# Performance work log

Hardware: AMD Instinct MI355X
Metric: run time of the kernel (lower is better)

The kernel has to match this reference:

```python
import jax, jax.numpy as jnp
import numpy as np

B, C_IN, H, W = 4, 256, 64, 64
LATENT = 256


def setup_inputs() -> dict:
    key = jax.random.key(0)
    ks = jax.random.split(key, 12)
    s_in = 1.0 / np.sqrt(C_IN)
    s_lat = 1.0 / np.sqrt(LATENT)
    return {
        "x": jax.random.normal(ks[0], (B, C_IN, H, W), dtype=jnp.float32),
        # 1x1 conv weights stored as [out, in]
        "wq": jax.random.normal(ks[1], (LATENT, C_IN), dtype=jnp.float32) * s_in,
        "bq": jnp.zeros((LATENT,), dtype=jnp.float32),
        "wk": jax.random.normal(ks[2], (LATENT, C_IN), dtype=jnp.float32) * s_in,
        "bk": jnp.zeros((LATENT,), dtype=jnp.float32),
        "wv": jax.random.normal(ks[3], (LATENT, C_IN), dtype=jnp.float32) * s_in,
        "bv": jnp.zeros((LATENT,), dtype=jnp.float32),
        "w_out": jax.random.normal(ks[4], (C_IN, LATENT), dtype=jnp.float32) * s_lat,
        "b_out": jnp.zeros((C_IN,), dtype=jnp.float32),
        # positional-embedding MLP (torch nn.Linear: y = x @ W.T + b)
        "mlp_w1": jax.random.normal(ks[5], (LATENT, LATENT), dtype=jnp.float32) * s_lat,
        "mlp_b1": jnp.zeros((LATENT,), dtype=jnp.float32),
        "mlp_w2": jax.random.normal(ks[6], (LATENT, LATENT), dtype=jnp.float32) * s_lat,
        "mlp_b2": jnp.zeros((LATENT,), dtype=jnp.float32),
    }


def _sinusoidal_table(timesteps, dim):
    # embed[t, d] = sin(arg) if d even else cos(arg), arg = t / 10000**(2d/dim)
    t = jnp.arange(timesteps, dtype=jnp.float32)[:, None]
    p = jnp.arange(dim, dtype=jnp.float32)[None, :]
    w = t / jnp.power(jnp.float32(10000.0), 2.0 * p / dim)
    even = (jnp.arange(dim) % 2 == 0)[None, :]
    return jnp.where(even, jnp.sin(w), jnp.cos(w))  # [T, dim]


def _conv1x1(x, w, b):
    # x: [B, Cin, H, W], w: [Cout, Cin]
    return jnp.einsum('bchw,oc->bohw', x, w) + b[None, :, None, None]


def reference(x, wq, bq, wk, bk, wv, bv, w_out, b_out, mlp_w1, mlp_b1, mlp_w2, mlp_b2):
    batch, _, h, w_ = x.shape
    L = wq.shape[0]
    hw = h * w_

    q = _conv1x1(x, wq, bq)
    k = _conv1x1(x, wk, bk)
    v = _conv1x1(x, wv, bv)

    pe = _sinusoidal_table(hw, L)                     # [HW, L]
    pe = jax.nn.silu(pe @ mlp_w1.T + mlp_b1) @ mlp_w2.T + mlp_b2
    pe = pe.reshape(1, L, h, w_)                      # faithful to torch reshape

    q = (q + pe).reshape(batch, L, hw)
    k = (k + pe).reshape(batch, L, hw)
    v = (v + pe).reshape(batch, L, hw)

    # attention[b, i, j] = sum_c q[b, c, i] * k[b, c, j] / sqrt(L)
    att = jnp.einsum('bci,bcj->bij', q, k) / jnp.sqrt(jnp.float32(L))
    att = jax.nn.softmax(att, axis=1)                 # SAGAN-style: softmax over queries
    res = jnp.einsum('bci,bij->bcj', v, att)          # bmm(v, attention)
    res = res.reshape(batch, L, h, w_)
    return _conv1x1(res, w_out, b_out)
```

## Files before the change

kernel.cpp:

```cpp
#include <hip/hip_runtime.h>
#include <cstdint>


typedef short s8v __attribute__((ext_vector_type(8)));
typedef float f32x4 __attribute__((ext_vector_type(4)));
typedef unsigned int u32x2 __attribute__((ext_vector_type(2)));
typedef unsigned int u32x4 __attribute__((ext_vector_type(4)));

#define DEVI static __device__ __forceinline__

DEVI unsigned short f2bf(float f) {
  union { float f; uint32_t u; } x; x.f = f;
  uint32_t u = x.u;
  return (unsigned short)((u + 0x7fffu + ((u >> 16) & 1u)) >> 16);
}

DEVI void pl32swap(uint32_t& a, uint32_t& b) {
#if __has_builtin(__builtin_amdgcn_permlane32_swap)
  u32x2 r = __builtin_amdgcn_permlane32_swap(a, b, false, false);
  a = r[0]; b = r[1];
#else
  asm("v_permlane32_swap_b32 %0, %1" : "+v"(a), "+v"(b));
#endif
}

DEVI void gl_lds16(const void* g, void* l) {
  __builtin_amdgcn_global_load_lds(
      (const __attribute__((address_space(1))) void*)g,
      (__attribute__((address_space(3))) void*)l,
      16, 0, 0);
}

DEVI void stage(const unsigned short* src, int ld, unsigned short* lds, int t) {
  gl_lds16(src + (long)(t >> 2) * ld + (t & 3) * 8, lds + (t >> 6) * 512);
}

template <int OBF, int BIAS, int PEM, int SILU>
__global__ __launch_bounds__(256) void gemm_nt(
    const unsigned short* __restrict__ A, const unsigned short* __restrict__ B,
    void* __restrict__ Cp, int K, int N, int ld, long sA, long sB, long sC,
    const float* __restrict__ bias, const float* __restrict__ pe, float scale) {
  const int bz = blockIdx.z;
  const unsigned short* Ab = A + (long)bz * sA;
  const unsigned short* Bb = B + (long)bz * sB;
  const int m0 = blockIdx.x * 128, n0 = blockIdx.y * 128;
  __shared__ __align__(16) unsigned short As[4096], Bs[4096];
  const int t = threadIdx.x;
  const int wave = t >> 6, lane = t & 63;
  const int wr = wave >> 1, wc = wave & 1;

  f32x4 acc[4][4];
#pragma unroll
  for (int i = 0; i < 4; i++)
#pragma unroll
    for (int j = 0; j < 4; j++) acc[i][j] = f32x4{0.f, 0.f, 0.f, 0.f};

  const int rl = lane & 15, kp = (lane >> 4) * 8;

  for (int k0 = 0; k0 < K; k0 += 32) {
    stage(Ab + (long)m0 * ld + k0, ld, As, t);
    stage(Ab + (long)(m0 + 64) * ld + k0, ld, As + 2048, t);
    stage(Bb + (long)n0 * ld + k0, ld, Bs, t);
    stage(Bb + (long)(n0 + 64) * ld + k0, ld, Bs + 2048, t);
    __syncthreads();

    s8v af[4], bfr[4];
#pragma unroll
    for (int i = 0; i < 4; i++)
      af[i] = *(const s8v*)(As + (wr * 64 + i * 16 + rl) * 32 + kp);
#pragma unroll
    for (int j = 0; j < 4; j++)
      bfr[j] = *(const s8v*)(Bs + (wc * 64 + j * 16 + rl) * 32 + kp);
#pragma unroll
    for (int i = 0; i < 4; i++)
#pragma unroll
      for (int j = 0; j < 4; j++)
        acc[i][j] = __builtin_amdgcn_mfma_f32_16x16x32_bf16(af[i], bfr[j],
                                                            acc[i][j], 0, 0, 0);
    __syncthreads();
  }

  const long cb = (long)bz * sC;
#pragma unroll
  for (int i = 0; i < 4; i++) {
    const int r0 = m0 + wr * 64 + i * 16 + (lane >> 4) * 4;
#pragma unroll
    for (int j = 0; j < 4; j++) {
      const int col = n0 + wc * 64 + j * 16 + (lane & 15);
#pragma unroll
      for (int r = 0; r < 4; r++) {
        const int row = r0 + r;
        float val = acc[i][j][r] * scale;
        if (BIAS == 1) val += bias[row];
        if (BIAS == 2) val += bias[col];
        if (PEM == 1) val += pe[(long)row * 4096 + col];
        if (PEM == 2) val += pe[(long)col * 4096 + row];
        if (SILU) val = val / (1.0f + __expf(-val));
        const long ci = cb + (long)row * N + col;
        if (OBF)
          ((unsigned short*)Cp)[ci] = f2bf(val);
        else
          ((float*)Cp)[ci] = val;
      }
    }
  }
}

__global__ __launch_bounds__(512) void gemm_qkv(
    const unsigned short* __restrict__ XT, const unsigned short* __restrict__ wqb,
    const unsigned short* __restrict__ wkb, const unsigned short* __restrict__ wvb,
    unsigned short* __restrict__ qT, unsigned short* __restrict__ kT,
    unsigned short* __restrict__ vB, const float* __restrict__ bq,
    const float* __restrict__ bk, const float* __restrict__ bv,
    const float* __restrict__ pe) {
  const int bz = blockIdx.z;
  const unsigned short* Ab = XT + (long)bz * 1048576;
  const int m0 = blockIdx.x * 128, n0 = blockIdx.y * 128;
  __shared__ __align__(16) unsigned short As[4096], Bq[4096], Bk[4096],
      Bv[4096];
  const int t = threadIdx.x;
  const int wave = t >> 6, lane = t & 63;
  const int wm = wave >> 2, wn = wave & 3;
  const int rl = lane & 15, kp = (lane >> 4) * 8;
  const int th = t >> 8, tt = t & 255;

  f32x4 aq[4][2], ak[4][2], av[4][2];
#pragma unroll
  for (int i = 0; i < 4; i++)
#pragma unroll
    for (int j = 0; j < 2; j++) {
      aq[i][j] = f32x4{0.f, 0.f, 0.f, 0.f};
      ak[i][j] = f32x4{0.f, 0.f, 0.f, 0.f};
      av[i][j] = f32x4{0.f, 0.f, 0.f, 0.f};
    }

  for (int k0 = 0; k0 < 256; k0 += 32) {
    const long ro = (long)(th * 64) * 256 + k0;
    stage(Ab + (long)m0 * 256 + ro, 256, As + th * 2048, tt);
    stage(wqb + (long)n0 * 256 + ro, 256, Bq + th * 2048, tt);
    stage(wkb + (long)n0 * 256 + ro, 256, Bk + th * 2048, tt);
    stage(wvb + (long)n0 * 256 + ro, 256, Bv + th * 2048, tt);
    __syncthreads();

    s8v af[4], b0[2], b1[2], b2[2];
#pragma unroll
    for (int i = 0; i < 4; i++)
      af[i] = *(const s8v*)(As + (wm * 64 + i * 16 + rl) * 32 + kp);
#pragma unroll
    for (int j = 0; j < 2; j++) {
      b0[j] = *(const s8v*)(Bq + (wn * 32 + j * 16 + rl) * 32 + kp);
      b1[j] = *(const s8v*)(Bk + (wn * 32 + j * 16 + rl) * 32 + kp);
      b2[j] = *(const s8v*)(Bv + (wn * 32 + j * 16 + rl) * 32 + kp);
    }
#pragma unroll
    for (int i = 0; i < 4; i++)
#pragma unroll
      for (int j = 0; j < 2; j++) {
        aq[i][j] = __builtin_amdgcn_mfma_f32_16x16x32_bf16(af[i], b0[j],
                                                           aq[i][j], 0, 0, 0);
        ak[i][j] = __builtin_amdgcn_mfma_f32_16x16x32_bf16(af[i], b1[j],
                                                           ak[i][j], 0, 0, 0);
        av[i][j] = __builtin_amdgcn_mfma_f32_16x16x32_bf16(af[i], b2[j],
                                                           av[i][j], 0, 0, 0);
      }
    __syncthreads();
  }

  const long cb = (long)bz * 1048576;
#pragma unroll
  for (int i = 0; i < 4; i++) {
    const int row0 = m0 + wm * 64 + i * 16 + (lane >> 4) * 4;
#pragma unroll
    for (int j = 0; j < 2; j++) {
      const int col = n0 + wn * 32 + j * 16 + rl;
      const float4 p4 = *(const float4*)(pe + (long)col * 4096 + row0);
      const float bqc = bq[col], bkc = bk[col], bvc = bv[col];
      ushort4 vpk;
      const float pv[4] = {p4.x, p4.y, p4.z, p4.w};
#pragma unroll
      for (int r = 0; r < 4; r++) {
        const int row = row0 + r;
        qT[cb + (long)row * 256 + col] = f2bf(aq[i][j][r] + bqc + pv[r]);
        kT[cb + (long)row * 256 + col] = f2bf(ak[i][j][r] + bkc + pv[r]);
      }
      vpk.x = f2bf(av[i][j][0] + bvc + pv[0]);
      vpk.y = f2bf(av[i][j][1] + bvc + pv[1]);
      vpk.z = f2bf(av[i][j][2] + bvc + pv[2]);
      vpk.w = f2bf(av[i][j][3] + bvc + pv[3]);
      *(ushort4*)(vB + cb + (long)col * 4096 + row0) = vpk;
    }
  }
}

__global__ __launch_bounds__(256) void gemm_out_f(
    const unsigned short* __restrict__ wob, const float* __restrict__ oPart,
    const float* __restrict__ lPart, const float* __restrict__ bo,
    float* __restrict__ out) {
  const int bz = blockIdx.z;
  const int m0 = blockIdx.x * 128, n0 = blockIdx.y * 128;
  __shared__ __align__(16) unsigned short As[4096], Bs[4096];
  const int t = threadIdx.x;
  const int wave = t >> 6, lane = t & 63;
  const int wr = wave >> 1, wc = wave & 1;

  f32x4 acc[4][4];
#pragma unroll
  for (int i = 0; i < 4; i++)
#pragma unroll
    for (int j = 0; j < 4; j++) acc[i][j] = f32x4{0.f, 0.f, 0.f, 0.f};

  const int rl = lane & 15, kp = (lane >> 4) * 8;
  const int tr = t >> 2, tc8 = (t & 3) * 8;

  const int j0_ = n0 + tr, j1_ = n0 + 64 + tr;
  const float* l0p = lPart + (long)(bz * 2) * 4096;
  const float* l1p = lPart + (long)(bz * 2 + 1) * 4096;
  const float inv0 = 1.0f / (l0p[j0_] + l1p[j0_]);
  const float inv1 = 1.0f / (l0p[j1_] + l1p[j1_]);
  const float* oP0 = oPart + (long)(bz * 2) * 1048576;
  const float* oP1 = oPart + (long)(bz * 2 + 1) * 1048576;

  for (int k0 = 0; k0 < 256; k0 += 32) {
    stage(wob + (long)m0 * 256 + k0, 256, As, t);
    stage(wob + (long)(m0 + 64) * 256 + k0, 256, As + 2048, t);
#pragma unroll
    for (int h = 0; h < 2; h++) {
      const int j = h ? j1_ : j0_;
      const float inv = h ? inv1 : inv0;
      const float4* a4 = (const float4*)(oP0 + (long)j * 256 + k0 + tc8);
      const float4* d4 = (const float4*)(oP1 + (long)j * 256 + k0 + tc8);
      const float4 a0 = a4[0], a1 = a4[1], d0 = d4[0], d1 = d4[1];
      s8v pk;
      pk[0] = (short)f2bf((a0.x + d0.x) * inv);
      pk[1] = (short)f2bf((a0.y + d0.y) * inv);
      pk[2] = (short)f2bf((a0.z + d0.z) * inv);
      pk[3] = (short)f2bf((a0.w + d0.w) * inv);
      pk[4] = (short)f2bf((a1.x + d1.x) * inv);
      pk[5] = (short)f2bf((a1.y + d1.y) * inv);
      pk[6] = (short)f2bf((a1.z + d1.z) * inv);
      pk[7] = (short)f2bf((a1.w + d1.w) * inv);
      *(s8v*)(Bs + h * 2048 + tr * 32 + tc8) = pk;
    }
    __syncthreads();

    s8v af[4], bfr[4];
#pragma unroll
    for (int i = 0; i < 4; i++)
      af[i] = *(const s8v*)(As + (wr * 64 + i * 16 + rl) * 32 + kp);
#pragma unroll
    for (int j = 0; j < 4; j++)
      bfr[j] = *(const s8v*)(Bs + (wc * 64 + j * 16 + rl) * 32 + kp);
#pragma unroll
    for (int i = 0; i < 4; i++)
#pragma unroll
      for (int j = 0; j < 4; j++)
        acc[i][j] = __builtin_amdgcn_mfma_f32_16x16x32_bf16(af[i], bfr[j],
                                                            acc[i][j], 0, 0, 0);
    __syncthreads();
  }

  const long cb = (long)bz * 1048576;
#pragma unroll
  for (int i = 0; i < 4; i++) {
    const int r0 = m0 + wr * 64 + i * 16 + (lane >> 4) * 4;
#pragma unroll
    for (int j = 0; j < 4; j++) {
      const int col = n0 + wc * 64 + j * 16 + (lane & 15);
#pragma unroll
      for (int r = 0; r < 4; r++) {
        const int row = r0 + r;
        out[cb + (long)row * 4096 + col] = acc[i][j][r] + bo[row];
      }
    }
  }
}

__global__ __launch_bounds__(512, 2) void flash_attn(
    const unsigned short* __restrict__ qTp, const unsigned short* __restrict__ kTp,
    const unsigned short* __restrict__ vBp, float* __restrict__ oPart,
    float* __restrict__ lPart) {
  const int bid = blockIdx.x;
  const int xcd = bid & 7;
  const int b = xcd >> 1, ihalf = xcd & 1;
  const int j0 = (bid >> 3) * 128;
  const long S = 1048576;
  const long ibase = (long)ihalf * 2048;
  const unsigned short* q = qTp + (long)b * S;
  const unsigned short* k = kTp + (long)b * S;
  const unsigned short* v = vBp + (long)b * S;
  const int ob = b * 2 + ihalf;

  __shared__ __align__(16) unsigned char ldsb[131584];

  const int t = threadIdx.x;
  const int wave = t >> 6, lane = t & 63;
  const int jq = wave & 3, ch = wave >> 2;
  const int rl = lane & 15, g = lane >> 4;
  const int kp = g * 8;
  const int ksw = ((g ^ ((rl >> 1) & 3)) << 3);
  const int qrow = (rl & 3) | ((rl & 4) << 1) | ((rl & 8) >> 1);
  const int kswq = ((g ^ ((qrow >> 1) & 3)) << 3);
  const int th = t >> 8, tt = t & 255;

  const unsigned short* krow = k + (long)(j0 + jq * 32 + rl) * 256 + kp;
  s8v kreg[2][8];
#pragma unroll
  for (int jf = 0; jf < 2; jf++)
#pragma unroll
    for (int s = 0; s < 8; s++)
      kreg[jf][s] = *(const s8v*)(krow + jf * 16 * 256 + s * 32);

  f32x4 oacc[16][2];
#pragma unroll
  for (int cf = 0; cf < 16; cf++)
#pragma unroll
    for (int jf = 0; jf < 2; jf++) oacc[cf][jf] = f32x4{0.f, 0.f, 0.f, 0.f};
  float plsum[2] = {0.f, 0.f};

  const int tr = tt >> 2, tc = tt & 3;
  const int sc = (tc ^ ((tr >> 1) & 3)) * 8;
  const unsigned short* qsrc[4];
  const unsigned short* vsrc[4];
  const int dsto = (tt >> 6) * 512;
#pragma unroll
  for (int ss = 0; ss < 4; ss++) {
    const int s_ = ss * 2 + th;
    qsrc[ss] = q + ibase * 256 + s_ * 32 + (long)tr * 256 + sc;
    vsrc[ss] = v + (long)((s_ >> 1) * 64) * 4096 + ibase + (s_ & 1) * 32 +
               (long)tr * 4096 + sc;
  }

#define STAGE_QV(bufsel)                                                     \
  {                                                                          \
    unsigned short* qD = (unsigned short*)(ldsb + ((bufsel) << 15));         \
    unsigned short* vD = (unsigned short*)(ldsb + 65536 + ((bufsel) << 15)); \
    _Pragma("unroll") for (int ss = 0; ss < 4; ss++) {                       \
      const int s_ = ss * 2 + th;                                            \
      gl_lds16(qsrc[ss], qD + s_ * 2048 + dsto);                             \
      gl_lds16(vsrc[ss], vD + s_ * 2048 + dsto);                             \
      qsrc[ss] += 16384;                                                     \
      vsrc[ss] += 64;                                                        \
    }                                                                        \
  }

  STAGE_QV(0)

  for (int n = 0; n < 32; ++n) {
    const int cur = n & 1;
    __syncthreads();
    STAGE_QV(cur ^ 1)

    f32x4 sa[2][2];
#pragma unroll
    for (int kk = 0; kk < 2; kk++)
#pragma unroll
      for (int jf = 0; jf < 2; jf++) sa[kk][jf] = f32x4{0.f, 0.f, 0.f, 0.f};
    const unsigned short* qbase =
        (const unsigned short*)(ldsb + (cur << 15)) +
        (ch * 32 + qrow) * 32 + kswq;
#pragma unroll
    for (int s = 0; s < 8; s++) {
      s8v qf0 = *(const s8v*)(qbase + s * 2048);
      s8v qf1 = *(const s8v*)(qbase + s * 2048 + 512);
      sa[0][0] = __builtin_amdgcn_mfma_f32_16x16x32_bf16(qf0, kreg[0][s],
                                                         sa[0][0], 0, 0, 0);
      sa[0][1] = __builtin_amdgcn_mfma_f32_16x16x32_bf16(qf0, kreg[1][s],
                                                         sa[0][1], 0, 0, 0);
      sa[1][0] = __builtin_amdgcn_mfma_f32_16x16x32_bf16(qf1, kreg[0][s],
                                                         sa[1][0], 0, 0, 0);
      sa[1][1] = __builtin_amdgcn_mfma_f32_16x16x32_bf16(qf1, kreg[1][s],
                                                         sa[1][1], 0, 0, 0);
    }

    uint32_t pd[2][2][2];
#pragma unroll
    for (int kk = 0; kk < 2; kk++)
#pragma unroll
      for (int jf = 0; jf < 2; jf++) {
        const float p0 = exp2f(sa[kk][jf][0] * 0.09016844005556021f);
        const float p1 = exp2f(sa[kk][jf][1] * 0.09016844005556021f);
        const float p2 = exp2f(sa[kk][jf][2] * 0.09016844005556021f);
        const float p3 = exp2f(sa[kk][jf][3] * 0.09016844005556021f);
        plsum[jf] += (p0 + p1) + (p2 + p3);
        pd[kk][jf][0] = (uint32_t)f2bf(p0) | ((uint32_t)f2bf(p1) << 16);
        pd[kk][jf][1] = (uint32_t)f2bf(p2) | ((uint32_t)f2bf(p3) << 16);
      }

    s8v pB[2];
#pragma unroll
    for (int jf = 0; jf < 2; jf++) {
      uint32_t a0 = pd[0][jf][0], b0 = pd[1][jf][0];
      uint32_t a1 = pd[0][jf][1], b1 = pd[1][jf][1];
      pl32swap(a0, b0);
      pl32swap(a1, b1);
      u32x4 w4 = {a0, a1, b0, b1};
      pB[jf] = __builtin_bit_cast(s8v, w4);
    }

    const unsigned short* vbase =
        (const unsigned short*)(ldsb + 65536 + (cur << 15)) + ch * 2048 +
        rl * 32 + ksw;
#pragma unroll
    for (int cf = 0; cf < 16; cf++) {
      s8v vb = *(const s8v*)(vbase + (cf >> 2) * 4096 + (cf & 3) * 512);
      oacc[cf][0] = __builtin_amdgcn_mfma_f32_16x16x32_bf16(vb, pB[0],
                                                            oacc[cf][0], 0, 0, 0);
      oacc[cf][1] = __builtin_amdgcn_mfma_f32_16x16x32_bf16(vb, pB[1],
                                                            oacc[cf][1], 0, 0, 0);
    }
  }

#pragma unroll
  for (int jf = 0; jf < 2; jf++) {
    plsum[jf] += __shfl_xor(plsum[jf], 16);
    plsum[jf] += __shfl_xor(plsum[jf], 32);
  }

  __syncthreads();
  float4* ex = (float4*)ldsb;
  float* exl = (float*)(ldsb + 131072);
  if (ch == 1) {
#pragma unroll
    for (int jf = 0; jf < 2; jf++) {
#pragma unroll
      for (int cf = 0; cf < 16; cf++)
        ex[jq * 2048 + (jf * 16 + rl) * 64 + cf * 4 + g] =
            float4{oacc[cf][jf][0], oacc[cf][jf][1], oacc[cf][jf][2],
                   oacc[cf][jf][3]};
      if (g == 0) exl[jq * 32 + jf * 16 + rl] = plsum[jf];
    }
  }
  __syncthreads();
  if (ch == 0) {
    float4* op4 = (float4*)(oPart + (long)ob * 1048576);
#pragma unroll
    for (int jf = 0; jf < 2; jf++) {
      const int jl = jq * 32 + jf * 16 + rl;
      if (g == 0)
        lPart[(long)ob * 4096 + j0 + jl] = plsum[jf] + exl[jl];
#pragma unroll
      for (int cf = 0; cf < 16; cf++) {
        const float4 o = ex[jq * 2048 + (jf * 16 + rl) * 64 + cf * 4 + g];
        op4[(long)(j0 + jl) * 64 + cf * 4 + g] =
            float4{oacc[cf][jf][0] + o.x, oacc[cf][jf][1] + o.y,
                   oacc[cf][jf][2] + o.z, oacc[cf][jf][3] + o.w};
      }
    }
  }
#undef STAGE_QV
}

__global__ __launch_bounds__(256) void prep_all(
    const float* __restrict__ a0, const float* __restrict__ a1,
    const float* __restrict__ a2, const float* __restrict__ a3,
    const float* __restrict__ a4, const float* __restrict__ a5,
    unsigned short* __restrict__ wdst, unsigned short* __restrict__ emb,
    const float* __restrict__ x, unsigned short* __restrict__ xt) {
  __shared__ float tile[32][33];
  const int bid = blockIdx.x;
  const int t = threadIdx.x;
  if (bid < 1536) {
    int idx = bid * 256 + t;
    int m = idx >> 16, r = idx & 65535;
    const float* s;
    switch (m) {
      case 0: s = a0; break;
      case 1: s = a1; break;
      case 2: s = a2; break;
      case 3: s = a3; break;
      case 4: s = a4; break;
      default: s = a5; break;
    }
    wdst[idx] = f2bf(s[r]);
  } else if (bid < 5632) {
    int idx = (bid - 1536) * 256 + t;
    int tt_ = idx >> 8, d = idx & 255;
    float freq = exp2f((float)d * -0.10381025296573598f);
    float w = (float)tt_ * freq;
    float sn, cs;
    __sincosf(w, &sn, &cs);
    emb[idx] = f2bf((d & 1) ? cs : sn);
  } else {
    const int bid2 = bid - 5632;
    const int s0 = (bid2 & 127) * 32, c0 = ((bid2 >> 7) & 7) * 32;
    const int b = bid2 >> 10;
    const int tx = t & 31, ty = t >> 5;
    const float* xb = x + (long)b * 256 * 4096;
#pragma unroll
    for (int r = 0; r < 32; r += 8)
      tile[ty + r][tx] = xb[(long)(c0 + ty + r) * 4096 + s0 + tx];
    __syncthreads();
    unsigned short* xtb = xt + (long)b * 4096 * 256;
#pragma unroll
    for (int r = 0; r < 32; r += 8)
      xtb[(long)(s0 + ty + r) * 256 + c0 + tx] = f2bf(tile[tx][ty + r]);
  }
}

extern "C" void kernel_launch(void* const* d_in, const int* in_sizes, int n_in,
                              void* d_out, int out_size, void* d_ws,
                              size_t ws_size, hipStream_t stream) {
  const float* x  = (const float*)d_in[0];
  const float* wq = (const float*)d_in[1];
  const float* bq = (const float*)d_in[2];
  const float* wk = (const float*)d_in[3];
  const float* bk = (const float*)d_in[4];
  const float* wv = (const float*)d_in[5];
  const float* bv = (const float*)d_in[6];
  const float* wo = (const float*)d_in[7];
  const float* bo = (const float*)d_in[8];
  const float* w1 = (const float*)d_in[9];
  const float* b1 = (const float*)d_in[10];
  const float* w2 = (const float*)d_in[11];
  const float* b2 = (const float*)d_in[12];
  float* out = (float*)d_out;

  char* ws = (char*)d_ws;
  unsigned short* wqb = (unsigned short*)(ws + 0);
  unsigned short* wkb = (unsigned short*)(ws + 131072);
  unsigned short* wvb = (unsigned short*)(ws + 262144);
  unsigned short* wob = (unsigned short*)(ws + 393216);
  unsigned short* w1b = (unsigned short*)(ws + 524288);
  unsigned short* w2b = (unsigned short*)(ws + 655360);
  unsigned short* emb = (unsigned short*)(ws + 786432);
  unsigned short* h1b = (unsigned short*)(ws + 2883584);
  float*          peF = (float*)(ws + 4980736);
  unsigned short* XT  = (unsigned short*)(ws + 9175040);
  unsigned short* qT  = (unsigned short*)(ws + 17563648);
  unsigned short* kT  = (unsigned short*)(ws + 25952256);
  unsigned short* vB  = (unsigned short*)(ws + 34340864);
  float*          oP  = (float*)(ws + 51118080);
  float*          lP  = (float*)(ws + 84672512);
  (void)ws_size; (void)in_sizes; (void)n_in; (void)out_size;

  const dim3 B256(256);

  prep_all<<<9728, B256, 0, stream>>>(wq, wk, wv, wo, w1, w2, wqb, emb, x, XT);
  gemm_nt<1, 2, 0, 1><<<dim3(32, 2, 1), B256, 0, stream>>>(
      emb, w1b, h1b, 256, 256, 256, 0, 0, 0, b1, nullptr, 1.0f);
  gemm_nt<0, 2, 0, 0><<<dim3(32, 2, 1), B256, 0, stream>>>(
      h1b, w2b, peF, 256, 256, 256, 0, 0, 0, b2, nullptr, 1.0f);
  gemm_qkv<<<dim3(32, 2, 4), dim3(512), 0, stream>>>(
      XT, wqb, wkb, wvb, qT, kT, vB, bq, bk, bv, peF);
  flash_attn<<<256, dim3(512), 0, stream>>>(qT, kT, vB, oP, lP);
  gemm_out_f<<<dim3(2, 32, 4), B256, 0, stream>>>(wob, oP, lP, bo, out);
}
```

Baseline: 148.6 us.

## Route attention probabilities through LDS instead of permlane swaps; retile output GEMM

```diff
diff --git a/kernel.cpp b/kernel.cpp
--- a/kernel.cpp
+++ b/kernel.cpp
@@ -4,8 +4,6 @@
 
 typedef short s8v __attribute__((ext_vector_type(8)));
 typedef float f32x4 __attribute__((ext_vector_type(4)));
-typedef unsigned int u32x2 __attribute__((ext_vector_type(2)));
-typedef unsigned int u32x4 __attribute__((ext_vector_type(4)));
 
 #define DEVI static __device__ __forceinline__
 
@@ -13,15 +11,6 @@
   union { float f; uint32_t u; } x; x.f = f;
   uint32_t u = x.u;
   return (unsigned short)((u + 0x7fffu + ((u >> 16) & 1u)) >> 16);
-}
-
-DEVI void pl32swap(uint32_t& a, uint32_t& b) {
-#if __has_builtin(__builtin_amdgcn_permlane32_swap)
-  u32x2 r = __builtin_amdgcn_permlane32_swap(a, b, false, false);
-  a = r[0]; b = r[1];
-#else
-  asm("v_permlane32_swap_b32 %0, %1" : "+v"(a), "+v"(b));
-#endif
 }
 
 DEVI void gl_lds16(const void* g, void* l) {
@@ -197,38 +186,33 @@
     const float* __restrict__ lPart, const float* __restrict__ bo,
     float* __restrict__ out) {
   const int bz = blockIdx.z;
-  const int m0 = blockIdx.x * 128, n0 = blockIdx.y * 128;
-  __shared__ __align__(16) unsigned short As[4096], Bs[4096];
+  const int n0 = blockIdx.y * 64;
+  __shared__ __align__(16) unsigned short As[8192], Bs[2048];
   const int t = threadIdx.x;
   const int wave = t >> 6, lane = t & 63;
-  const int wr = wave >> 1, wc = wave & 1;
-
-  f32x4 acc[4][4];
-#pragma unroll
-  for (int i = 0; i < 4; i++)
-#pragma unroll
-    for (int j = 0; j < 4; j++) acc[i][j] = f32x4{0.f, 0.f, 0.f, 0.f};
-
   const int rl = lane & 15, kp = (lane >> 4) * 8;
   const int tr = t >> 2, tc8 = (t & 3) * 8;
 
-  const int j0_ = n0 + tr, j1_ = n0 + 64 + tr;
+  f32x4 acc[4][4];
+#pragma unroll
+  for (int i = 0; i < 4; i++)
+#pragma unroll
+    for (int j = 0; j < 4; j++) acc[i][j] = f32x4{0.f, 0.f, 0.f, 0.f};
+
+  const int j_ = n0 + tr;
   const float* l0p = lPart + (long)(bz * 2) * 4096;
   const float* l1p = lPart + (long)(bz * 2 + 1) * 4096;
-  const float inv0 = 1.0f / (l0p[j0_] + l1p[j0_]);
-  const float inv1 = 1.0f / (l0p[j1_] + l1p[j1_]);
+  const float inv = 1.0f / (l0p[j_] + l1p[j_]);
   const float* oP0 = oPart + (long)(bz * 2) * 1048576;
   const float* oP1 = oPart + (long)(bz * 2 + 1) * 1048576;
 
   for (int k0 = 0; k0 < 256; k0 += 32) {
-    stage(wob + (long)m0 * 256 + k0, 256, As, t);
-    stage(wob + (long)(m0 + 64) * 256 + k0, 256, As + 2048, t);
-#pragma unroll
-    for (int h = 0; h < 2; h++) {
-      const int j = h ? j1_ : j0_;
-      const float inv = h ? inv1 : inv0;
-      const float4* a4 = (const float4*)(oP0 + (long)j * 256 + k0 + tc8);
-      const float4* d4 = (const float4*)(oP1 + (long)j * 256 + k0 + tc8);
+#pragma unroll
+    for (int s_ = 0; s_ < 4; s_++)
+      stage(wob + (long)(s_ * 64) * 256 + k0, 256, As + s_ * 2048, t);
+    {
+      const float4* a4 = (const float4*)(oP0 + (long)j_ * 256 + k0 + tc8);
+      const float4* d4 = (const float4*)(oP1 + (long)j_ * 256 + k0 + tc8);
       const float4 a0 = a4[0], a1 = a4[1], d0 = d4[0], d1 = d4[1];
       s8v pk;
       pk[0] = (short)f2bf((a0.x + d0.x) * inv);
@@ -239,17 +223,17 @@
       pk[5] = (short)f2bf((a1.y + d1.y) * inv);
       pk[6] = (short)f2bf((a1.z + d1.z) * inv);
       pk[7] = (short)f2bf((a1.w + d1.w) * inv);
-      *(s8v*)(Bs + h * 2048 + tr * 32 + tc8) = pk;
+      *(s8v*)(Bs + tr * 32 + tc8) = pk;
     }
     __syncthreads();
 
     s8v af[4], bfr[4];
 #pragma unroll
     for (int i = 0; i < 4; i++)
-      af[i] = *(const s8v*)(As + (wr * 64 + i * 16 + rl) * 32 + kp);
+      af[i] = *(const s8v*)(As + (wave * 64 + i * 16 + rl) * 32 + kp);
 #pragma unroll
     for (int j = 0; j < 4; j++)
-      bfr[j] = *(const s8v*)(Bs + (wc * 64 + j * 16 + rl) * 32 + kp);
+      bfr[j] = *(const s8v*)(Bs + (j * 16 + rl) * 32 + kp);
 #pragma unroll
     for (int i = 0; i < 4; i++)
 #pragma unroll
@@ -262,10 +246,10 @@
   const long cb = (long)bz * 1048576;
 #pragma unroll
   for (int i = 0; i < 4; i++) {
-    const int r0 = m0 + wr * 64 + i * 16 + (lane >> 4) * 4;
+    const int r0 = wave * 64 + i * 16 + (lane >> 4) * 4;
 #pragma unroll
     for (int j = 0; j < 4; j++) {
-      const int col = n0 + wc * 64 + j * 16 + (lane & 15);
+      const int col = n0 + j * 16 + (lane & 15);
 #pragma unroll
       for (int r = 0; r < 4; r++) {
         const int row = r0 + r;
@@ -290,7 +274,7 @@
   const unsigned short* v = vBp + (long)b * S;
   const int ob = b * 2 + ihalf;
 
-  __shared__ __align__(16) unsigned char ldsb[131584];
+  __shared__ __align__(16) unsigned char ldsb[151552];
 
   const int t = threadIdx.x;
   const int wave = t >> 6, lane = t & 63;
@@ -298,9 +282,9 @@
   const int rl = lane & 15, g = lane >> 4;
   const int kp = g * 8;
   const int ksw = ((g ^ ((rl >> 1) & 3)) << 3);
-  const int qrow = (rl & 3) | ((rl & 4) << 1) | ((rl & 8) >> 1);
-  const int kswq = ((g ^ ((qrow >> 1) & 3)) << 3);
   const int th = t >> 8, tt = t & 255;
+  unsigned short* pL = (unsigned short*)(ldsb + 131072);
+  unsigned short* pLw = pL + wave * 1280;
 
   const unsigned short* krow = k + (long)(j0 + jq * 32 + rl) * 256 + kp;
   s8v kreg[2][8];
@@ -310,12 +294,12 @@
     for (int s = 0; s < 8; s++)
       kreg[jf][s] = *(const s8v*)(krow + jf * 16 * 256 + s * 32);
 
-  f32x4 oacc[16][2];
-#pragma unroll
-  for (int cf = 0; cf < 16; cf++)
-#pragma unroll
-    for (int jf = 0; jf < 2; jf++) oacc[cf][jf] = f32x4{0.f, 0.f, 0.f, 0.f};
-  float plsum[2] = {0.f, 0.f};
+  f32x4 oacc[2][16];
+#pragma unroll
+  for (int jf = 0; jf < 2; jf++)
+#pragma unroll
+    for (int cf = 0; cf < 16; cf++) oacc[jf][cf] = f32x4{0.f, 0.f, 0.f, 0.f};
+  float plsum[2][4] = {{0.f, 0.f, 0.f, 0.f}, {0.f, 0.f, 0.f, 0.f}};
 
   const int tr = tt >> 2, tc = tt & 3;
   const int sc = (tc ^ ((tr >> 1) & 3)) * 8;
@@ -338,8 +322,8 @@
       const int s_ = ss * 2 + th;                                            \
       gl_lds16(qsrc[ss], qD + s_ * 2048 + dsto);                             \
       gl_lds16(vsrc[ss], vD + s_ * 2048 + dsto);                             \
-      qsrc[ss] += 16384;                                                     \
-      vsrc[ss] += 64;                                                        \
+      qsrc[ss] += 16384;                     \
+      vsrc[ss] += 64;                        \
     }                                                                        \
   }
 
@@ -348,103 +332,104 @@
   for (int n = 0; n < 32; ++n) {
     const int cur = n & 1;
     __syncthreads();
-    STAGE_QV(cur ^ 1)
+    if (n + 1 < 32) STAGE_QV(cur ^ 1)
+
+    const unsigned short* qLb = (const unsigned short*)(ldsb + (cur << 15));
+    const unsigned short* vLb =
+        (const unsigned short*)(ldsb + 65536 + (cur << 15));
 
     f32x4 sa[2][2];
 #pragma unroll
-    for (int kk = 0; kk < 2; kk++)
-#pragma unroll
-      for (int jf = 0; jf < 2; jf++) sa[kk][jf] = f32x4{0.f, 0.f, 0.f, 0.f};
-    const unsigned short* qbase =
-        (const unsigned short*)(ldsb + (cur << 15)) +
-        (ch * 32 + qrow) * 32 + kswq;
+    for (int jf = 0; jf < 2; jf++)
+#pragma unroll
+      for (int f = 0; f < 2; f++) sa[jf][f] = f32x4{0.f, 0.f, 0.f, 0.f};
+    const unsigned short* qbase = qLb + (ch * 32 + rl) * 32 + ksw;
 #pragma unroll
     for (int s = 0; s < 8; s++) {
-      s8v qf0 = *(const s8v*)(qbase + s * 2048);
-      s8v qf1 = *(const s8v*)(qbase + s * 2048 + 512);
-      sa[0][0] = __builtin_amdgcn_mfma_f32_16x16x32_bf16(qf0, kreg[0][s],
-                                                         sa[0][0], 0, 0, 0);
-      sa[0][1] = __builtin_amdgcn_mfma_f32_16x16x32_bf16(qf0, kreg[1][s],
-                                                         sa[0][1], 0, 0, 0);
-      sa[1][0] = __builtin_amdgcn_mfma_f32_16x16x32_bf16(qf1, kreg[0][s],
-                                                         sa[1][0], 0, 0, 0);
-      sa[1][1] = __builtin_amdgcn_mfma_f32_16x16x32_bf16(qf1, kreg[1][s],
-                                                         sa[1][1], 0, 0, 0);
-    }
-
-    uint32_t pd[2][2][2];
-#pragma unroll
-    for (int kk = 0; kk < 2; kk++)
-#pragma unroll
-      for (int jf = 0; jf < 2; jf++) {
-        const float p0 = exp2f(sa[kk][jf][0] * 0.09016844005556021f);
-        const float p1 = exp2f(sa[kk][jf][1] * 0.09016844005556021f);
-        const float p2 = exp2f(sa[kk][jf][2] * 0.09016844005556021f);
-        const float p3 = exp2f(sa[kk][jf][3] * 0.09016844005556021f);
-        plsum[jf] += (p0 + p1) + (p2 + p3);
-        pd[kk][jf][0] = (uint32_t)f2bf(p0) | ((uint32_t)f2bf(p1) << 16);
-        pd[kk][jf][1] = (uint32_t)f2bf(p2) | ((uint32_t)f2bf(p3) << 16);
-      }
-
-    s8v pB[2];
-#pragma unroll
-    for (int jf = 0; jf < 2; jf++) {
-      uint32_t a0 = pd[0][jf][0], b0 = pd[1][jf][0];
-      uint32_t a1 = pd[0][jf][1], b1 = pd[1][jf][1];
-      pl32swap(a0, b0);
-      pl32swap(a1, b1);
-      u32x4 w4 = {a0, a1, b0, b1};
-      pB[jf] = __builtin_bit_cast(s8v, w4);
-    }
-
-    const unsigned short* vbase =
-        (const unsigned short*)(ldsb + 65536 + (cur << 15)) + ch * 2048 +
-        rl * 32 + ksw;
+#pragma unroll
+      for (int f = 0; f < 2; f++) {
+        s8v bf = *(const s8v*)(qbase + s * 2048 + f * 512);
+        sa[0][f] = __builtin_amdgcn_mfma_f32_16x16x32_bf16(kreg[0][s], bf,
+                                                           sa[0][f], 0, 0, 0);
+        sa[1][f] = __builtin_amdgcn_mfma_f32_16x16x32_bf16(kreg[1][s], bf,
+                                                           sa[1][f], 0, 0, 0);
+      }
+    }
+
+#pragma unroll
+    for (int jf = 0; jf < 2; jf++)
+#pragma unroll
+      for (int f = 0; f < 2; f++)
+#pragma unroll
+        for (int r = 0; r < 4; r++) {
+          const float p = __expf(sa[jf][f][r] * 0.0625f);
+          plsum[jf][r] += p;
+          pLw[jf * 640 + (g * 4 + r) * 40 + f * 16 + rl] = f2bf(p);
+        }
+
+    s8v pa0 = *(const s8v*)(pLw + rl * 40 + kp);
+    s8v pa1 = *(const s8v*)(pLw + 640 + rl * 40 + kp);
+    const unsigned short* vbase = vLb + ch * 2048 + rl * 32 + ksw;
 #pragma unroll
     for (int cf = 0; cf < 16; cf++) {
       s8v vb = *(const s8v*)(vbase + (cf >> 2) * 4096 + (cf & 3) * 512);
-      oacc[cf][0] = __builtin_amdgcn_mfma_f32_16x16x32_bf16(vb, pB[0],
-                                                            oacc[cf][0], 0, 0, 0);
-      oacc[cf][1] = __builtin_amdgcn_mfma_f32_16x16x32_bf16(vb, pB[1],
-                                                            oacc[cf][1], 0, 0, 0);
-    }
-  }
-
-#pragma unroll
-  for (int jf = 0; jf < 2; jf++) {
-    plsum[jf] += __shfl_xor(plsum[jf], 16);
-    plsum[jf] += __shfl_xor(plsum[jf], 32);
-  }
+      oacc[0][cf] = __builtin_amdgcn_mfma_f32_16x16x32_bf16(pa0, vb,
+                                                            oacc[0][cf], 0, 0, 0);
+      oacc[1][cf] = __builtin_amdgcn_mfma_f32_16x16x32_bf16(pa1, vb,
+                                                            oacc[1][cf], 0, 0, 0);
+    }
+  }
+
+#pragma unroll
+  for (int jf = 0; jf < 2; jf++)
+#pragma unroll
+    for (int r = 0; r < 4; r++) {
+      plsum[jf][r] += __shfl_xor(plsum[jf][r], 1);
+      plsum[jf][r] += __shfl_xor(plsum[jf][r], 2);
+      plsum[jf][r] += __shfl_xor(plsum[jf][r], 4);
+      plsum[jf][r] += __shfl_xor(plsum[jf][r], 8);
+    }
 
   __syncthreads();
-  float4* ex = (float4*)ldsb;
+  float* ex = (float*)ldsb;
   float* exl = (float*)(ldsb + 131072);
   if (ch == 1) {
+    float* exw = ex + jq * 8192;
 #pragma unroll
     for (int jf = 0; jf < 2; jf++) {
 #pragma unroll
       for (int cf = 0; cf < 16; cf++)
-        ex[jq * 2048 + (jf * 16 + rl) * 64 + cf * 4 + g] =
-            float4{oacc[cf][jf][0], oacc[cf][jf][1], oacc[cf][jf][2],
-                   oacc[cf][jf][3]};
-      if (g == 0) exl[jq * 32 + jf * 16 + rl] = plsum[jf];
+#pragma unroll
+        for (int r = 0; r < 4; r++)
+          exw[(jf * 16 + g * 4 + r) * 256 + cf * 16 + rl] = oacc[jf][cf][r];
+      if (rl == 0) {
+#pragma unroll
+        for (int r = 0; r < 4; r++)
+          exl[jq * 32 + jf * 16 + g * 4 + r] = plsum[jf][r];
+      }
     }
   }
   __syncthreads();
   if (ch == 0) {
-    float4* op4 = (float4*)(oPart + (long)ob * 1048576);
+    float* exw = ex + jq * 8192;
+    float* op = oPart + (long)ob * 1048576;
 #pragma unroll
     for (int jf = 0; jf < 2; jf++) {
-      const int jl = jq * 32 + jf * 16 + rl;
-      if (g == 0)
-        lPart[(long)ob * 4096 + j0 + jl] = plsum[jf] + exl[jl];
-#pragma unroll
-      for (int cf = 0; cf < 16; cf++) {
-        const float4 o = ex[jq * 2048 + (jf * 16 + rl) * 64 + cf * 4 + g];
-        op4[(long)(j0 + jl) * 64 + cf * 4 + g] =
-            float4{oacc[cf][jf][0] + o.x, oacc[cf][jf][1] + o.y,
-                   oacc[cf][jf][2] + o.z, oacc[cf][jf][3] + o.w};
-      }
+      if (rl == 0) {
+#pragma unroll
+        for (int r = 0; r < 4; r++) {
+          const int jl = jq * 32 + jf * 16 + g * 4 + r;
+          lPart[(long)ob * 4096 + j0 + jl] = plsum[jf][r] + exl[jl];
+        }
+      }
+#pragma unroll
+      for (int cf = 0; cf < 16; cf++)
+#pragma unroll
+        for (int r = 0; r < 4; r++) {
+          const int jl2 = jf * 16 + g * 4 + r;
+          op[(long)(j0 + jq * 32 + jl2) * 256 + cf * 16 + rl] =
+              oacc[jf][cf][r] + exw[jl2 * 256 + cf * 16 + rl];
+        }
     }
   }
 #undef STAGE_QV
@@ -543,5 +528,5 @@
   gemm_qkv<<<dim3(32, 2, 4), dim3(512), 0, stream>>>(
       XT, wqb, wkb, wvb, qT, kT, vB, bq, bk, bv, peF);
   flash_attn<<<256, dim3(512), 0, stream>>>(qT, kT, vB, oP, lP);
-  gemm_out_f<<<dim3(2, 32, 4), B256, 0, stream>>>(wob, oP, lP, bo, out);
-}
+  gemm_out_f<<<dim3(1, 64, 4), B256, 0, stream>>>(wob, oP, lP, bo, out);
+}
```

Measured after the change: 144.6 us. 1.03x faster.
